# Performance work log

Measured on AMD Instinct MI355X. Metric: run time of the kernel, lower is better.

Reference implementation:

```python
import jax, jax.numpy as jnp
import numpy as np

N_NODES = 100000
N_EDGES = 500000
N_REL = 6
IN_DIM = 64
HID = 128
HEADS = 4
C = HID // HEADS  # 32 per-head channels
N_GRAPHS = 1024
EPS = 1e-16


def setup_inputs() -> dict:
    key = jax.random.key(0)
    ks = jax.random.split(key, 20)
    x = jax.random.normal(ks[0], (N_NODES, IN_DIM), dtype=jnp.float32)
    edge_index = jax.random.randint(ks[1], (N_REL, 2, N_EDGES), 0, N_NODES, dtype=jnp.int64)
    batch = jnp.sort(jax.random.randint(ks[2], (N_NODES,), 0, N_GRAPHS, dtype=jnp.int64))
    s = 0.02
    return {
        "x": x, "edge_index": edge_index, "batch": batch,
        # layer1 GAT params (stacked over 6 relations)
        "W1": jax.random.normal(ks[3], (N_REL, IN_DIM, HID), dtype=jnp.float32) * s,
        "as1": jax.random.normal(ks[4], (N_REL, HEADS, C), dtype=jnp.float32) * s,
        "ad1": jax.random.normal(ks[5], (N_REL, HEADS, C), dtype=jnp.float32) * s,
        "b1": jnp.zeros((N_REL, HID), dtype=jnp.float32),
        # layer2 GAT params
        "W2": jax.random.normal(ks[6], (N_REL, HID, HID), dtype=jnp.float32) * s,
        "as2": jax.random.normal(ks[7], (N_REL, HEADS, C), dtype=jnp.float32) * s,
        "ad2": jax.random.normal(ks[8], (N_REL, HEADS, C), dtype=jnp.float32) * s,
        "b2": jnp.zeros((N_REL, HID), dtype=jnp.float32),
        # layernorms
        "g1": jnp.ones((HID,), dtype=jnp.float32), "be1": jnp.zeros((HID,), dtype=jnp.float32),
        "g2": jnp.ones((HID,), dtype=jnp.float32), "be2": jnp.zeros((HID,), dtype=jnp.float32),
        # attention pooling query + output proj
        "q": jax.random.normal(ks[9], (HID,), dtype=jnp.float32) * s,
        "Wp": jax.random.normal(ks[10], (HID, HID), dtype=jnp.float32) * s,
        "bp": jnp.zeros((HID,), dtype=jnp.float32),
    }


def _gat_hetero_layer(x, edge_index, W, a_src, a_dst, b):
    # HeteroConv(aggr='sum') over R GATConv relations, add_self_loops=False, eval (no dropout)
    N = x.shape[0]
    out = jnp.zeros((N, HEADS * C), dtype=x.dtype)
    for r in range(N_REL):
        h = (x @ W[r]).reshape(N, HEADS, C)          # [N,H,C]
        al_s = (h * a_src[r]).sum(-1)                # [N,H]
        al_d = (h * a_dst[r]).sum(-1)                # [N,H]
        src, dst = edge_index[r, 0], edge_index[r, 1]
        e = jax.nn.leaky_relu(al_s[src] + al_d[dst], 0.2)   # [E,H]
        m = jax.ops.segment_max(e, dst, num_segments=N)
        ex = jnp.exp(e - m[dst])
        den = jax.ops.segment_sum(ex, dst, num_segments=N)
        alpha = ex / (den[dst] + EPS)                # segment softmax over incoming edges
        msg = h[src] * alpha[:, :, None]             # [E,H,C]
        agg = jax.ops.segment_sum(msg, dst, num_segments=N).reshape(N, HEADS * C)
        out = out + agg + b[r]
    return out


def _layernorm(x, g, b):
    mu = x.mean(-1, keepdims=True)
    v = ((x - mu) ** 2).mean(-1, keepdims=True)
    return (x - mu) * jax.lax.rsqrt(v + 1e-5) * g + b


def _softsign(x):
    return x / (1.0 + jnp.abs(x))


def reference(x, edge_index, batch, W1, as1, ad1, b1, W2, as2, ad2, b2,
              g1, be1, g2, be2, q, Wp, bp):
    h = _gat_hetero_layer(x, edge_index, W1, as1, ad1, b1)
    h = _layernorm(_softsign(h), g1, be1)
    h = _gat_hetero_layer(h, edge_index, W2, as2, ad2, b2)
    h = _layernorm(_softsign(h), g2, be2)
    # attention pooling: segment softmax over batch, then weighted scatter-sum
    scores = (h * q).sum(-1)                                   # [N]
    m = jax.ops.segment_max(scores, batch, num_segments=N_GRAPHS)
    ex = jnp.exp(scores - m[batch])
    den = jax.ops.segment_sum(ex, batch, num_segments=N_GRAPHS)
    w = ex / (den[batch] + EPS)
    pooled = jax.ops.segment_sum(h * w[:, None], batch, num_segments=N_GRAPHS)  # [G,HID]
    return pooled @ Wp + bp
```

## Files before the change

### kernel.cpp

```cpp
#include <hip/hip_runtime.h>
#include <hip/hip_bf16.h>
#include <hip/hip_fp16.h>

#define N_NODES_C 100000
#define N_EDGES_C 500000
#define N_REL_C 6
#define IN_DIM_C 64
#define HID_C 128
#define HEADS_C 4
#define CPH_C 32
#define N_GRAPHS_C 1024
#define NBLK_SCAN 391

typedef _Float16 f16x8 __attribute__((ext_vector_type(8)));
typedef float f32x4 __attribute__((ext_vector_type(4)));

__global__ __launch_bounds__(256) void hist_rank_convert_kernel(
    const int* __restrict__ ei, int* __restrict__ cnt, int* __restrict__ rank,
    const float* __restrict__ x, __half* __restrict__ xh,
    const float* __restrict__ W1, const float* __restrict__ W2,
    __half* __restrict__ Wt1, __half* __restrict__ Wt2) {
    int i = blockIdx.x * 256 + threadIdx.x;
    if (i < N_NODES_C * IN_DIM_C / 4) {
        float4 v = ((const float4*)x)[i];
        union { __half h[4]; uint2 u; } u;
        u.h[0] = __float2half(v.x); u.h[1] = __float2half(v.y);
        u.h[2] = __float2half(v.z); u.h[3] = __float2half(v.w);
        ((uint2*)xh)[i] = u.u;
    }
    if (i < N_REL_C * IN_DIM_C * HID_C) {
        int r = i / (IN_DIM_C * HID_C);
        int rem = i - r * (IN_DIM_C * HID_C);
        int k = rem / HID_C, n = rem - k * HID_C;
        Wt1[(size_t)r * HID_C * IN_DIM_C + n * IN_DIM_C + k] = __float2half(W1[i]);
    }
    if (i < N_REL_C * HID_C * HID_C) {
        int r = i / (HID_C * HID_C);
        int rem = i - r * (HID_C * HID_C);
        int k = rem / HID_C, n = rem - k * HID_C;
        Wt2[(size_t)r * HID_C * HID_C + n * HID_C + k] = __float2half(W2[i]);
    }
    if (i < N_REL_C * N_EDGES_C) {
        int r = i / N_EDGES_C;
        int e = i - r * N_EDGES_C;
        int dst = ei[(size_t)r * 2 * N_EDGES_C + N_EDGES_C + e];
        rank[i] = atomicAdd(&cnt[r * N_NODES_C + dst], 1);
    }
}

__global__ __launch_bounds__(256) void scan1_kernel(const int* __restrict__ cnt,
                                                    int* __restrict__ rowptr,
                                                    int* __restrict__ blocksums) {
    int r = blockIdx.y, b = blockIdx.x, t = threadIdx.x;
    int idx = b * 256 + t;
    int v = (idx < N_NODES_C) ? cnt[r * N_NODES_C + idx] : 0;
    int orig = v;
    int lane = t & 63, w = t >> 6;
#pragma unroll
    for (int off = 1; off < 64; off <<= 1) {
        int n = __shfl_up(v, off);
        if (lane >= off) v += n;
    }
    __shared__ int wt[4];
    if (lane == 63) wt[w] = v;
    __syncthreads();
    int add = 0;
    for (int i = 0; i < w; i++) add += wt[i];
    v += add;
    if (idx < N_NODES_C) rowptr[(size_t)r * (N_NODES_C + 1) + idx] = v - orig;
    if (t == 255) blocksums[r * NBLK_SCAN + b] = v;
}

__global__ __launch_bounds__(512) void scan2_kernel(int* __restrict__ blocksums) {
    int r = blockIdx.x, t = threadIdx.x;
    int v = (t < NBLK_SCAN) ? blocksums[r * NBLK_SCAN + t] : 0;
    int orig = v;
    int lane = t & 63, w = t >> 6;
#pragma unroll
    for (int off = 1; off < 64; off <<= 1) {
        int n = __shfl_up(v, off);
        if (lane >= off) v += n;
    }
    __shared__ int wt[8];
    if (lane == 63) wt[w] = v;
    __syncthreads();
    int add = 0;
    for (int i = 0; i < w; i++) add += wt[i];
    v += add;
    if (t < NBLK_SCAN) blocksums[r * NBLK_SCAN + t] = v - orig;
}

__global__ __launch_bounds__(256) void scatter_kernel(const int* __restrict__ ei,
                                                      const int* __restrict__ rowptrP,
                                                      const int* __restrict__ bsums,
                                                      const int* __restrict__ rank,
                                                      int* __restrict__ srcids) {
    int i = blockIdx.x * 256 + threadIdx.x;
    if (i >= N_REL_C * N_EDGES_C) return;
    int r = i / N_EDGES_C;
    int e = i - r * N_EDGES_C;
    int src = ei[(size_t)r * 2 * N_EDGES_C + e];
    int dst = ei[(size_t)r * 2 * N_EDGES_C + N_EDGES_C + e];
    int base = rowptrP[(size_t)r * (N_NODES_C + 1) + dst] + bsums[r * NBLK_SCAN + (dst >> 8)];
    srcids[(size_t)r * N_EDGES_C + base + rank[i]] = src;
}

template <int K>
__global__ __launch_bounds__(256) void gemm_mfma_kernel(
    const __half* __restrict__ Xh, const __half* __restrict__ Wtbase,
    __half* __restrict__ Hbase,
    const float* __restrict__ asbase, const float* __restrict__ adbase,
    float* __restrict__ alsbase, float* __restrict__ aldbase) {
    __shared__ _Float16 Bsh[128][K + 8];
    __shared__ float lgb[4][2][16][4];
    const int slot = blockIdx.y;
    const __half* Wt = Wtbase + (size_t)slot * HID_C * K;
    __half* H = Hbase + (size_t)slot * N_NODES_C * HID_C;
    const int tid = threadIdx.x;
    const int wave = tid >> 6, lane = tid & 63;
    const int m = lane & 15, quad = lane >> 4;

    constexpr int CPR = K / 8;
    constexpr int NCHUNK = 128 * CPR;
#pragma unroll
    for (int j = 0; j < NCHUNK / 256; j++) {
        int chunk = tid + j * 256;
        int n = chunk / CPR;
        int kc = (chunk - n * CPR) * 8;
        *(uint4*)&Bsh[n][kc] = *(const uint4*)(Wt + (size_t)n * K + kc);
    }
    __syncthreads();

    const int r0 = blockIdx.x * 64 + wave * 16;
    int arow = r0 + m;
    if (arow > N_NODES_C - 1) arow = N_NODES_C - 1;
    const __half* ap = Xh + (size_t)arow * K + quad * 8;

    f32x4 acc[8];
#pragma unroll
    for (int t = 0; t < 8; t++) acc[t] = (f32x4){0.f, 0.f, 0.f, 0.f};

#pragma unroll
    for (int kc = 0; kc < K; kc += 32) {
        f16x8 a = *(const f16x8*)(ap + kc);
#pragma unroll
        for (int t = 0; t < 8; t++) {
            f16x8 b = *(const f16x8*)&Bsh[t * 16 + m][kc + quad * 8];
            acc[t] = __builtin_amdgcn_mfma_f32_16x16x32_f16(a, b, acc[t], 0, 0, 0);
        }
    }
    __syncthreads();

    _Float16* trp = &Bsh[0][0] + wave * (16 * 136);
#pragma unroll
    for (int t = 0; t < 8; t++)
#pragma unroll
        for (int i = 0; i < 4; i++)
            trp[(quad * 4 + i) * 136 + t * 16 + m] = (_Float16)acc[t][i];
#pragma unroll
    for (int p = 0; p < 4; p++) {
        int idx = p * 512 + lane * 8;
        int row = idx >> 7;
        int col = idx & 127;
        int R = r0 + row;
        if (R < N_NODES_C)
            *(uint4*)(H + (size_t)R * HID_C + col) = *(const uint4*)&trp[row * 136 + col];
    }

    const float* a_s = asbase + slot * HID_C;
    const float* a_d = adbase + slot * HID_C;
    float* als = alsbase + (size_t)slot * N_NODES_C * HEADS_C;
    float* ald = aldbase + (size_t)slot * N_NODES_C * HEADS_C;
    float ps[4][4], pd[4][4];
#pragma unroll
    for (int h = 0; h < 4; h++) {
        float as0 = a_s[h * 32 + m], as1 = a_s[h * 32 + 16 + m];
        float ad0 = a_d[h * 32 + m], ad1 = a_d[h * 32 + 16 + m];
#pragma unroll
        for (int i = 0; i < 4; i++) {
            ps[h][i] = acc[2 * h][i] * as0 + acc[2 * h + 1][i] * as1;
            pd[h][i] = acc[2 * h][i] * ad0 + acc[2 * h + 1][i] * ad1;
        }
    }
#pragma unroll
    for (int off = 1; off < 16; off <<= 1) {
#pragma unroll
        for (int h = 0; h < 4; h++)
#pragma unroll
            for (int i = 0; i < 4; i++) {
                ps[h][i] += __shfl_xor(ps[h][i], off);
                pd[h][i] += __shfl_xor(pd[h][i], off);
            }
    }
#pragma unroll
    for (int h = 0; h < 4; h++) {
        if (m == h) {
#pragma unroll
            for (int i = 0; i < 4; i++) {
                lgb[wave][0][quad * 4 + i][h] = ps[h][i];
                lgb[wave][1][quad * 4 + i][h] = pd[h][i];
            }
        }
    }
    {
        int row = lane & 15;
        int which = lane >> 4;
        if (which < 2) {
            int R = r0 + row;
            if (R < N_NODES_C) {
                float4 v = *(const float4*)&lgb[wave][which][row][0];
                float* dst = which ? ald : als;
                *(float4*)(dst + (size_t)R * HEADS_C) = v;
            }
        }
    }
}

__global__ __launch_bounds__(256) void csr_agg_kernel(
    const int* __restrict__ rowptrP, const int* __restrict__ bsums,
    const int* __restrict__ srcids,
    const __half* __restrict__ A, const float* __restrict__ als,
    const float* __restrict__ ald, int rel_start, int rel_cnt,
    const float* __restrict__ bias, int first, int last,
    float* __restrict__ B,
    const float* __restrict__ g, const float* __restrict__ be,
    __half* __restrict__ Cbh) {
    int node = blockIdx.x * 4 + (threadIdx.x >> 6);
    int lane = threadIdx.x & 63;
    int grp = lane >> 4;
    int j16 = lane & 15;
    int head = j16 >> 2;
    int cbase = j16 * 8;

    float acc[8];
    if (first) {
#pragma unroll
        for (int t = 0; t < 8; t++) {
            float s = 0.f;
#pragma unroll
            for (int r = 0; r < N_REL_C; r++) s += bias[r * HID_C + cbase + t];
            acc[t] = s;
        }
    } else {
        float4 b0 = *(const float4*)(B + (size_t)node * HID_C + cbase);
        float4 b1 = *(const float4*)(B + (size_t)node * HID_C + cbase + 4);
        acc[0] = b0.x; acc[1] = b0.y; acc[2] = b0.z; acc[3] = b0.w;
        acc[4] = b1.x; acc[5] = b1.y; acc[6] = b1.z; acc[7] = b1.w;
    }

    for (int j = 0; j < rel_cnt; j++) {
        int r = rel_start + j;
        const int* rp = rowptrP + (size_t)r * (N_NODES_C + 1);
        const int* bs = bsums + r * NBLK_SCAN;
        const int* sp = srcids + (size_t)r * N_EDGES_C;
        const __half* Aj = A + (size_t)j * N_NODES_C * HID_C;
        const float* alj = als + (size_t)j * N_NODES_C * HEADS_C;
        float aldv = ald[(size_t)j * N_NODES_C * HEADS_C + node * HEADS_C + head];
        int s = rp[node] + bs[node >> 8];
        int e = (node == N_NODES_C - 1) ? N_EDGES_C
                                        : rp[node + 1] + bs[(node + 1) >> 8];
        float racc[8];
#pragma unroll
        for (int t = 0; t < 8; t++) racc[t] = 0.f;
        float rden = 0.f;

        union HU { uint4 u; _Float16 h[8]; };
        int i = s + grp;
        int src = (i < e) ? sp[i] : 0;
        HU rw; rw.u = *(const uint4*)(Aj + (size_t)src * HID_C + cbase);
        float lg = alj[src * HEADS_C + head];
        for (; i < e; i += 4) {
            int nsrc = (i + 4 < e) ? sp[i + 4] : 0;
            HU nrw; nrw.u = *(const uint4*)(Aj + (size_t)nsrc * HID_C + cbase);
            float nlg = alj[nsrc * HEADS_C + head];
            float v = lg + aldv;
            v = fmaxf(v, 0.2f * v);
            float ex = __expf(v);
            rden += ex;
#pragma unroll
            for (int t = 0; t < 8; t++)
                racc[t] = fmaf((float)rw.h[t], ex, racc[t]);
            src = nsrc; rw = nrw; lg = nlg;
        }
#pragma unroll
        for (int off = 16; off < 64; off <<= 1) {
            rden += __shfl_xor(rden, off);
#pragma unroll
            for (int t = 0; t < 8; t++) racc[t] += __shfl_xor(racc[t], off);
        }
        float inv = 1.f / (rden + 1e-16f);
#pragma unroll
        for (int t = 0; t < 8; t++) acc[t] = fmaf(racc[t], inv, acc[t]);
    }

    if (!last) {
        if (grp == 0) {
            float4 o0 = make_float4(acc[0], acc[1], acc[2], acc[3]);
            float4 o1 = make_float4(acc[4], acc[5], acc[6], acc[7]);
            *(float4*)(B + (size_t)node * HID_C + cbase) = o0;
            *(float4*)(B + (size_t)node * HID_C + cbase + 4) = o1;
        }
    } else {
        float ss[8];
        float sum = 0.f, sq = 0.f;
#pragma unroll
        for (int t = 0; t < 8; t++) {
            float v = acc[t] / (1.f + fabsf(acc[t]));
            ss[t] = v;
            sum += v;
            sq = fmaf(v, v, sq);
        }
#pragma unroll
        for (int off = 1; off < 16; off <<= 1) {
            sum += __shfl_xor(sum, off);
            sq += __shfl_xor(sq, off);
        }
        float mu = sum * (1.f / 128.f);
        float var = sq * (1.f / 128.f) - mu * mu;
        float inv = rsqrtf(var + 1e-5f);
        if (grp == 0) {
            float4 gv0 = *(const float4*)(g + cbase);
            float4 gv1 = *(const float4*)(g + cbase + 4);
            float4 bv0 = *(const float4*)(be + cbase);
            float4 bv1 = *(const float4*)(be + cbase + 4);
            union { uint4 u; __half2 h2[4]; } ow;
            ow.h2[0] = __float22half2_rn(make_float2(
                (ss[0] - mu) * inv * gv0.x + bv0.x, (ss[1] - mu) * inv * gv0.y + bv0.y));
            ow.h2[1] = __float22half2_rn(make_float2(
                (ss[2] - mu) * inv * gv0.z + bv0.z, (ss[3] - mu) * inv * gv0.w + bv0.w));
            ow.h2[2] = __float22half2_rn(make_float2(
                (ss[4] - mu) * inv * gv1.x + bv1.x, (ss[5] - mu) * inv * gv1.y + bv1.y));
            ow.h2[3] = __float22half2_rn(make_float2(
                (ss[6] - mu) * inv * gv1.z + bv1.z, (ss[7] - mu) * inv * gv1.w + bv1.w));
            *(uint4*)(Cbh + (size_t)node * HID_C + cbase) = ow.u;
        }
    }
}

__device__ __forceinline__ int lower_bound_i(const int* __restrict__ a, int n, int v) {
    int lo = 0, hi = n;
    while (lo < hi) {
        int mid = (lo + hi) >> 1;
        if (a[mid] < v) lo = mid + 1; else hi = mid;
    }
    return lo;
}

__global__ __launch_bounds__(256) void pool_kernel(const __half* __restrict__ H,
                                                   const int* __restrict__ batch,
                                                   const float* __restrict__ q,
                                                   float* __restrict__ pooled) {
    int g = blockIdx.x;
    int t = threadIdx.x;
    int wave = t >> 6, lane = t & 63;
    int start = lower_bound_i(batch, N_NODES_C, g);
    int end = lower_bound_i(batch, N_NODES_C, g + 1);
    float q0 = q[lane * 2], q1 = q[lane * 2 + 1];
    float p0 = 0.f, p1 = 0.f, den = 0.f;
    for (int n = start + wave; n < end; n += 4) {
        float2 hv = __half22float2(*(const __half2*)(H + (size_t)n * HID_C + lane * 2));
        float part = hv.x * q0 + hv.y * q1;
#pragma unroll
        for (int off = 1; off < 64; off <<= 1) part += __shfl_xor(part, off);
        float exs = __expf(part);
        den += exs;
        p0 = fmaf(exs, hv.x, p0);
        p1 = fmaf(exs, hv.y, p1);
    }
    __shared__ float sp[4][HID_C];
    __shared__ float sden[4];
    sp[wave][lane * 2] = p0;
    sp[wave][lane * 2 + 1] = p1;
    if (lane == 0) sden[wave] = den;
    __syncthreads();
    if (wave == 0) {
        float a0 = sp[0][lane * 2] + sp[1][lane * 2] + sp[2][lane * 2] + sp[3][lane * 2];
        float a1 = sp[0][lane * 2 + 1] + sp[1][lane * 2 + 1] + sp[2][lane * 2 + 1] + sp[3][lane * 2 + 1];
        float d = sden[0] + sden[1] + sden[2] + sden[3];
        float w = 1.f / (d + 1e-16f);
        pooled[(size_t)g * HID_C + lane * 2] = a0 * w;
        pooled[(size_t)g * HID_C + lane * 2 + 1] = a1 * w;
    }
}

__global__ __launch_bounds__(128) void proj_kernel(const float* __restrict__ pooled,
                                                   const float* __restrict__ Wp,
                                                   const float* __restrict__ bp,
                                                   float* __restrict__ out) {
    int g = blockIdx.x, c = threadIdx.x;
    __shared__ float pl[HID_C];
    pl[c] = pooled[(size_t)g * HID_C + c];
    __syncthreads();
    float s = bp[c];
    for (int k = 0; k < HID_C; k++) s = fmaf(pl[k], Wp[k * HID_C + c], s);
    out[(size_t)g * HID_C + c] = s;
}

extern "C" void kernel_launch(void* const* d_in, const int* in_sizes, int n_in,
                              void* d_out, int out_size, void* d_ws, size_t ws_size,
                              hipStream_t stream) {
    const float* x   = (const float*)d_in[0];
    const int* ei    = (const int*)d_in[1];
    const int* batch = (const int*)d_in[2];
    const float* W1  = (const float*)d_in[3];
    const float* as1 = (const float*)d_in[4];
    const float* ad1 = (const float*)d_in[5];
    const float* b1  = (const float*)d_in[6];
    const float* W2  = (const float*)d_in[7];
    const float* as2 = (const float*)d_in[8];
    const float* ad2 = (const float*)d_in[9];
    const float* b2  = (const float*)d_in[10];
    const float* g1  = (const float*)d_in[11];
    const float* be1 = (const float*)d_in[12];
    const float* g2  = (const float*)d_in[13];
    const float* be2 = (const float*)d_in[14];
    const float* q   = (const float*)d_in[15];
    const float* Wp  = (const float*)d_in[16];
    const float* bp  = (const float*)d_in[17];
    float* out = (float*)d_out;

    const size_t NH = (size_t)N_NODES_C * HID_C;
    char* w = (char*)d_ws;
    __half* xh    = (__half*)w;   w += (size_t)N_NODES_C * IN_DIM_C * 2;
    __half* Cbh   = (__half*)w;   w += NH * 2;
    __half* Wt1   = (__half*)w;   w += (size_t)N_REL_C * IN_DIM_C * HID_C * 2;
    __half* Wt2   = (__half*)w;   w += (size_t)N_REL_C * HID_C * HID_C * 2;
    float* pooled = (float*)w;    w += (size_t)N_GRAPHS_C * HID_C * 4;
    int* rowptr   = (int*)w;      w += ((size_t)N_REL_C * (N_NODES_C + 1) * 4 + 15) & ~15ull;
    int* srcids   = (int*)w;      w += (size_t)N_REL_C * N_EDGES_C * 4;
    int* cnt      = (int*)w;      w += (size_t)N_REL_C * N_NODES_C * 4;
    int* bsums    = (int*)w;      w += ((size_t)N_REL_C * NBLK_SCAN * 4 + 15) & ~15ull;

    const size_t fixed_bytes = (size_t)(w - (char*)d_ws);
    const size_t slot_bytes = NH * 2 + 2 * (size_t)N_NODES_C * HEADS_C * 4;
    int nA = 1;
    float* B = nullptr;
    {
        size_t rem = (ws_size > fixed_bytes) ? (ws_size - fixed_bytes) : 0;
        size_t k = rem / slot_bytes;
        if (k >= 6) {
            nA = 6;
        } else {
            size_t rem2 = (rem > NH * 4) ? (rem - NH * 4) : 0;
            size_t k2 = rem2 / slot_bytes;
            nA = (int)(k2 < 1 ? 1 : (k2 > 5 ? 5 : k2));
        }
    }
    float* als = (float*)w;
    float* ald = als + (size_t)nA * N_NODES_C * HEADS_C;
    __half* A  = (__half*)(ald + (size_t)nA * N_NODES_C * HEADS_C);
    if (nA < 6) B = (float*)(A + (size_t)nA * NH);
    int* rank = (int*)A;

    hipMemsetAsync(cnt, 0, (size_t)N_REL_C * N_NODES_C * sizeof(int), stream);
    const int ehg = (N_REL_C * N_EDGES_C + 255) / 256;
    hist_rank_convert_kernel<<<ehg, 256, 0, stream>>>(ei, cnt, rank, x, xh, W1, W2, Wt1, Wt2);
    scan1_kernel<<<dim3(NBLK_SCAN, N_REL_C), 256, 0, stream>>>(cnt, rowptr, bsums);
    scan2_kernel<<<N_REL_C, 512, 0, stream>>>(bsums);
    scatter_kernel<<<ehg, 256, 0, stream>>>(ei, rowptr, bsums, rank, srcids);

    const int gemm_grid = (N_NODES_C + 63) / 64;
    const int agg_grid = N_NODES_C / 4;

    for (int gs = 0; gs < N_REL_C; gs += nA) {
        int c2 = (N_REL_C - gs) < nA ? (N_REL_C - gs) : nA;
        gemm_mfma_kernel<IN_DIM_C><<<dim3(gemm_grid, c2), 256, 0, stream>>>(
            xh, Wt1 + (size_t)gs * IN_DIM_C * HID_C, A,
            as1 + gs * HID_C, ad1 + gs * HID_C, als, ald);
        csr_agg_kernel<<<agg_grid, 256, 0, stream>>>(
            rowptr, bsums, srcids, A, als, ald, gs, c2,
            b1, (gs == 0) ? 1 : 0, (gs + c2 == N_REL_C) ? 1 : 0,
            B, g1, be1, Cbh);
    }
    for (int gs = 0; gs < N_REL_C; gs += nA) {
        int c2 = (N_REL_C - gs) < nA ? (N_REL_C - gs) : nA;
        gemm_mfma_kernel<HID_C><<<dim3(gemm_grid, c2), 256, 0, stream>>>(
            Cbh, Wt2 + (size_t)gs * HID_C * HID_C, A,
            as2 + gs * HID_C, ad2 + gs * HID_C, als, ald);
        csr_agg_kernel<<<agg_grid, 256, 0, stream>>>(
            rowptr, bsums, srcids, A, als, ald, gs, c2,
            b2, (gs == 0) ? 1 : 0, (gs + c2 == N_REL_C) ? 1 : 0,
            B, g2, be2, Cbh);
    }

    pool_kernel<<<N_GRAPHS_C, 256, 0, stream>>>(Cbh, batch, q, pooled);
    proj_kernel<<<N_GRAPHS_C, 128, 0, stream>>>(pooled, Wp, bp, out);
}
```

Before: 941.1 us.

## Split relations across lane groups instead of splitting edges within each relation

The CSR aggregation kernel now assigns each of the four 16-lane groups in a wavefront to a different relation, and each group walks all of that relation's in-edges serially. Before, all four groups split the edges of one relation and reduced with shuffles after every relation. This removes the per-relation cross-group shuffle reduction and its serialization, keeping only one final reduction. In exchange, each group's loop length now follows its relation's degree, so load imbalance across groups can grow, and lanes sit idle when the relation count is not a multiple of four.

```diff
diff --git a/kernel.cpp b/kernel.cpp
--- a/kernel.cpp
+++ b/kernel.cpp
@@ -232,45 +232,39 @@
     int head = j16 >> 2;
     int cbase = j16 * 8;
 
-    float acc[8];
-    if (first) {
-#pragma unroll
-        for (int t = 0; t < 8; t++) {
-            float s = 0.f;
-#pragma unroll
-            for (int r = 0; r < N_REL_C; r++) s += bias[r * HID_C + cbase + t];
-            acc[t] = s;
-        }
-    } else {
-        float4 b0 = *(const float4*)(B + (size_t)node * HID_C + cbase);
-        float4 b1 = *(const float4*)(B + (size_t)node * HID_C + cbase + 4);
-        acc[0] = b0.x; acc[1] = b0.y; acc[2] = b0.z; acc[3] = b0.w;
-        acc[4] = b1.x; acc[5] = b1.y; acc[6] = b1.z; acc[7] = b1.w;
-    }
-
-    for (int j = 0; j < rel_cnt; j++) {
-        int r = rel_start + j;
+    float accp[8];
+#pragma unroll
+    for (int t = 0; t < 8; t++) accp[t] = 0.f;
+
+    const int npass = (rel_cnt + 3) / 4;
+    for (int pass = 0; pass < npass; pass++) {
+        int j = pass * 4 + grp;
+        int active = (j < rel_cnt) ? 1 : 0;
+        int jj = active ? j : 0;
+        int r = rel_start + jj;
         const int* rp = rowptrP + (size_t)r * (N_NODES_C + 1);
         const int* bs = bsums + r * NBLK_SCAN;
         const int* sp = srcids + (size_t)r * N_EDGES_C;
-        const __half* Aj = A + (size_t)j * N_NODES_C * HID_C;
-        const float* alj = als + (size_t)j * N_NODES_C * HEADS_C;
-        float aldv = ald[(size_t)j * N_NODES_C * HEADS_C + node * HEADS_C + head];
+        const __half* Aj = A + (size_t)jj * N_NODES_C * HID_C;
+        const float* alj = als + (size_t)jj * N_NODES_C * HEADS_C;
+        float aldv = ald[(size_t)jj * N_NODES_C * HEADS_C + node * HEADS_C + head];
         int s = rp[node] + bs[node >> 8];
         int e = (node == N_NODES_C - 1) ? N_EDGES_C
                                         : rp[node + 1] + bs[(node + 1) >> 8];
+        if (!active) e = s;
+
         float racc[8];
 #pragma unroll
         for (int t = 0; t < 8; t++) racc[t] = 0.f;
         float rden = 0.f;
 
         union HU { uint4 u; _Float16 h[8]; };
-        int i = s + grp;
+        int i = s;
         int src = (i < e) ? sp[i] : 0;
         HU rw; rw.u = *(const uint4*)(Aj + (size_t)src * HID_C + cbase);
         float lg = alj[src * HEADS_C + head];
-        for (; i < e; i += 4) {
-            int nsrc = (i + 4 < e) ? sp[i + 4] : 0;
+        for (; i < e; i++) {
+            int nsrc = (i + 1 < e) ? sp[i + 1] : 0;
             HU nrw; nrw.u = *(const uint4*)(Aj + (size_t)nsrc * HID_C + cbase);
             float nlg = alj[nsrc * HEADS_C + head];
             float v = lg + aldv;
@@ -282,15 +276,33 @@
                 racc[t] = fmaf((float)rw.h[t], ex, racc[t]);
             src = nsrc; rw = nrw; lg = nlg;
         }
-#pragma unroll
-        for (int off = 16; off < 64; off <<= 1) {
-            rden += __shfl_xor(rden, off);
-#pragma unroll
-            for (int t = 0; t < 8; t++) racc[t] += __shfl_xor(racc[t], off);
-        }
         float inv = 1.f / (rden + 1e-16f);
 #pragma unroll
-        for (int t = 0; t < 8; t++) acc[t] = fmaf(racc[t], inv, acc[t]);
+        for (int t = 0; t < 8; t++) accp[t] = fmaf(racc[t], inv, accp[t]);
+    }
+
+#pragma unroll
+    for (int off = 16; off < 64; off <<= 1) {
+#pragma unroll
+        for (int t = 0; t < 8; t++) accp[t] += __shfl_xor(accp[t], off);
+    }
+
+    float acc[8];
+    if (first) {
+#pragma unroll
+        for (int t = 0; t < 8; t++) {
+            float sbias = 0.f;
+#pragma unroll
+            for (int r = 0; r < N_REL_C; r++) sbias += bias[r * HID_C + cbase + t];
+            acc[t] = sbias + accp[t];
+        }
+    } else {
+        float4 b0 = *(const float4*)(B + (size_t)node * HID_C + cbase);
+        float4 b1 = *(const float4*)(B + (size_t)node * HID_C + cbase + 4);
+        acc[0] = b0.x + accp[0]; acc[1] = b0.y + accp[1];
+        acc[2] = b0.z + accp[2]; acc[3] = b0.w + accp[3];
+        acc[4] = b1.x + accp[4]; acc[5] = b1.y + accp[5];
+        acc[6] = b1.z + accp[6]; acc[7] = b1.w + accp[7];
     }
 
     if (!last) {
```

Measured after the change: 940.7 us, median of 2. Within noise of the previous version (-0.0%).
